# Kernel optimization log

Hardware: AMD Instinct MI355X
Metric: run time of the kernel (lower is better)

Reference implementation:

```python
import jax, jax.numpy as jnp
import numpy as np

BETA = 2.0  # config.beta_start (beta_anneal=True, step 0)


def _generate_e8_roots() -> np.ndarray:
    roots = []
    # 112 integer roots: (+-1, +-1, 0^6) in all index pairs
    for i in range(8):
        for j in range(i + 1, 8):
            for si in (1.0, -1.0):
                for sj in (1.0, -1.0):
                    v = np.zeros(8, dtype=np.float32)
                    v[i] = si
                    v[j] = sj
                    roots.append(v)
    # 128 half-integer roots: (+-1/2)^8 with even number of minus signs
    for bits in range(256):
        signs = np.array([1.0 if ((bits >> k) & 1) == 0 else -1.0 for k in range(8)], dtype=np.float32)
        if int((signs < 0).sum()) % 2 == 0:
            roots.append(0.5 * signs)
    return np.stack(roots)  # [240, 8], each of norm sqrt(2)


def setup_inputs() -> dict:
    key = jax.random.key(0)
    ks = jax.random.split(key, 4)
    B, S, D_Q, H, D_K, N_SLOTS, D_V = 4, 65536, 14, 32, 8, 240, 256
    query = jax.random.normal(ks[0], (B, S, D_Q), dtype=jnp.float32)
    # orthogonal-ish init approximated with scaled gaussians (math path identical)
    W1 = jax.random.normal(ks[1], (H, D_Q), dtype=jnp.float32) * (1.0 / np.sqrt(D_Q))
    b1 = jnp.zeros((H,), dtype=jnp.float32)
    W2 = jax.random.normal(ks[2], (D_K, H), dtype=jnp.float32) * (1.0 / np.sqrt(H))
    b2 = jnp.zeros((D_K,), dtype=jnp.float32)
    values = jax.random.normal(ks[3], (N_SLOTS, D_V), dtype=jnp.float32) * 0.02
    roots = _generate_e8_roots()
    keys_n = jnp.asarray(roots / np.linalg.norm(roots, axis=-1, keepdims=True))
    return {"query": query, "W1": W1, "b1": b1, "W2": W2, "b2": b2,
            "values": values, "keys_n": keys_n}


def reference(query, W1, b1, W2, b2, values, keys_n):
    # flatten [B,S,D] -> [N,D] as in read()
    x = query.reshape(-1, query.shape[-1])
    # G2Projection: Linear(14,32) -> GELU (exact) -> Linear(32,8) -> L2 normalize
    h = jax.nn.gelu(x @ W1.T + b1, approximate=False)
    q8 = h @ W2.T + b2
    q8 = q8 / jnp.maximum(jnp.linalg.norm(q8, axis=-1, keepdims=True), 1e-12)
    # Hopfield attention over 240 normalized E8 root keys
    sim = q8 @ keys_n.T                      # [N, 240]
    attn = jax.nn.softmax(BETA * sim, axis=-1)
    content = attn @ values                  # [N, 256]
    return content, attn
```

## Files before the change

### kernel.cpp

```cpp
#include <hip/hip_runtime.h>
#include <math.h>

#define DQ 14
#define HD 32
#define DK 8
#define NK 240
#define DV 256
#define RB 64
#define NFRAG 65536

typedef __attribute__((ext_vector_type(8))) short bf16x8;
typedef __attribute__((ext_vector_type(4))) float f32x4;

__device__ __forceinline__ unsigned bf16_rn(float x) {
    unsigned u = __float_as_uint(x);
    return (u + 0x7fffu + ((u >> 16) & 1u)) >> 16;
}

__global__ void prep_values(const float* __restrict__ values,
                            unsigned short* __restrict__ ws_hi,
                            unsigned short* __restrict__ ws_lo) {
    int idx = blockIdx.x * 256 + threadIdx.x;
    int e  = idx & 7;
    int l  = (idx >> 3) & 63;
    int ks = (idx >> 9) & 7;
    int nt = idx >> 12;
    int k = ks * 32 + ((l >> 4) << 3) + e;
    int n = nt * 16 + (l & 15);
    float v = (k < NK) ? values[k * DV + n] : 0.0f;
    unsigned hb = bf16_rn(v);
    float hf = __uint_as_float(hb << 16);
    unsigned lb = bf16_rn(v - hf);
    ws_hi[idx] = (unsigned short)hb;
    ws_lo[idx] = (unsigned short)lb;
}

__global__ __launch_bounds__(256, 2)
void em_fused(const float* __restrict__ query,
              const float* __restrict__ W1, const float* __restrict__ b1,
              const float* __restrict__ W2, const float* __restrict__ b2,
              const float* __restrict__ keys,
              const unsigned short* __restrict__ ws_hi,
              const unsigned short* __restrict__ ws_lo,
              float* __restrict__ out_content, float* __restrict__ out_attn)
{
    __shared__ float s_x[RB][DQ];
    __shared__ float s_h[RB][HD + 1];
    __shared__ float s_q8[RB][DK + 1];
    __shared__ __align__(16) unsigned short s_Ah[RB * 256];
    __shared__ __align__(16) unsigned short s_Al[RB * 256];

    const int tid = threadIdx.x;
    const long row0 = (long)blockIdx.x * RB;

    for (int e = tid; e < RB * DQ; e += 256) {
        s_x[e / DQ][e % DQ] = query[row0 * DQ + e];
    }
    __syncthreads();

    #pragma unroll
    for (int it = 0; it < (RB * HD) / 256; ++it) {
        int task = it * 256 + tid;
        int r = task >> 5, j = task & 31;
        float acc = b1[j];
        #pragma unroll
        for (int c = 0; c < DQ; ++c) acc += s_x[r][c] * W1[j * DQ + c];
        s_h[r][j] = 0.5f * acc * (1.0f + erff(acc * 0.70710678118654752f));
    }
    __syncthreads();

    #pragma unroll
    for (int it = 0; it < (RB * DK) / 256; ++it) {
        int task = it * 256 + tid;
        int r = task >> 3, i = task & 7;
        float acc = b2[i];
        #pragma unroll
        for (int c = 0; c < HD; ++c) acc += s_h[r][c] * W2[i * HD + c];
        s_q8[r][i] = acc;
    }
    __syncthreads();

    if (tid < RB) {
        float ss = 0.f;
        #pragma unroll
        for (int i = 0; i < DK; ++i) { float v = s_q8[tid][i]; ss += v * v; }
        float inv = 1.0f / fmaxf(sqrtf(ss), 1e-12f);
        #pragma unroll
        for (int i = 0; i < DK; ++i) s_q8[tid][i] *= inv;
    }
    __syncthreads();

    {
        const int wv = tid >> 6, lane = tid & 63;
        const int t0 = lane * 4;
        float kr[4][DK];
        #pragma unroll
        for (int s = 0; s < 4; ++s) {
            #pragma unroll
            for (int c = 0; c < DK; ++c)
                kr[s][c] = (t0 + s < NK) ? keys[(t0 + s) * DK + c] : 0.0f;
        }
        char* ahp = (char*)s_Ah;
        char* alp = (char*)s_Al;
        for (int rr = 0; rr < 16; ++rr) {
            const int r = wv * 16 + rr;
            float q[DK];
            #pragma unroll
            for (int c = 0; c < DK; ++c) q[c] = s_q8[r][c];
            float ex[4];
            float ssum = 0.f;
            #pragma unroll
            for (int s = 0; s < 4; ++s) {
                float sim = 0.f;
                #pragma unroll
                for (int c = 0; c < DK; ++c) sim += q[c] * kr[s][c];
                float v = (t0 + s < NK) ? __expf(2.0f * sim) : 0.0f;
                ex[s] = v;
                ssum += v;
            }
            #pragma unroll
            for (int m = 1; m < 64; m <<= 1) ssum += __shfl_xor(ssum, m, 64);
            const float inv = 1.0f / ssum;
            float a0 = ex[0] * inv, a1 = ex[1] * inv, a2 = ex[2] * inv, a3 = ex[3] * inv;
            if (t0 < NK) {
                *(float4*)&out_attn[(row0 + r) * NK + t0] =
                    make_float4(a0, a1, a2, a3);
            }
            unsigned h0 = bf16_rn(a0), h1 = bf16_rn(a1), h2 = bf16_rn(a2), h3 = bf16_rn(a3);
            float f0 = __uint_as_float(h0 << 16), f1 = __uint_as_float(h1 << 16);
            float f2 = __uint_as_float(h2 << 16), f3 = __uint_as_float(h3 << 16);
            unsigned l0 = bf16_rn(a0 - f0), l1 = bf16_rn(a1 - f1);
            unsigned l2 = bf16_rn(a2 - f2), l3 = bf16_rn(a3 - f3);
            unsigned off = ((unsigned)(r * 512 + lane * 8)) ^ (((unsigned)(r & 7)) << 4);
            *(ushort4*)(ahp + off) = make_ushort4((unsigned short)h0, (unsigned short)h1,
                                                  (unsigned short)h2, (unsigned short)h3);
            *(ushort4*)(alp + off) = make_ushort4((unsigned short)l0, (unsigned short)l1,
                                                  (unsigned short)l2, (unsigned short)l3);
        }
    }
    __syncthreads();

    {
        const int wv = tid >> 6, lane = tid & 63;
        const int l15 = lane & 15, l4 = lane >> 4;
        f32x4 acc[4][4];
        #pragma unroll
        for (int i = 0; i < 4; ++i)
            #pragma unroll
            for (int j = 0; j < 4; ++j)
                acc[i][j] = (f32x4){0.f, 0.f, 0.f, 0.f};

        const char* ahp = (const char*)s_Ah;
        const char* alp = (const char*)s_Al;
        const bf16x8* Bh = (const bf16x8*)ws_hi;
        const bf16x8* Bl = (const bf16x8*)ws_lo;

        #pragma unroll
        for (int ks = 0; ks < 8; ++ks) {
            bf16x8 bh[4], bl[4], ah[4], al[4];
            #pragma unroll
            for (int ntl = 0; ntl < 4; ++ntl) {
                int fi = (((wv * 4 + ntl) * 8 + ks) << 6) + lane;
                bh[ntl] = Bh[fi];
                bl[ntl] = Bl[fi];
            }
            #pragma unroll
            for (int mt = 0; mt < 4; ++mt) {
                int m = mt * 16 + l15;
                unsigned off = ((unsigned)(m * 512 + ks * 64 + l4 * 16)) ^
                               (((unsigned)(m & 7)) << 4);
                ah[mt] = *(const bf16x8*)(ahp + off);
                al[mt] = *(const bf16x8*)(alp + off);
            }
            #pragma unroll
            for (int ntl = 0; ntl < 4; ++ntl) {
                #pragma unroll
                for (int mt = 0; mt < 4; ++mt) {
                    acc[mt][ntl] = __builtin_amdgcn_mfma_f32_16x16x32_bf16(
                        ah[mt], bh[ntl], acc[mt][ntl], 0, 0, 0);
                    acc[mt][ntl] = __builtin_amdgcn_mfma_f32_16x16x32_bf16(
                        al[mt], bh[ntl], acc[mt][ntl], 0, 0, 0);
                    acc[mt][ntl] = __builtin_amdgcn_mfma_f32_16x16x32_bf16(
                        ah[mt], bl[ntl], acc[mt][ntl], 0, 0, 0);
                }
            }
        }

        #pragma unroll
        for (int mt = 0; mt < 4; ++mt) {
            #pragma unroll
            for (int ntl = 0; ntl < 4; ++ntl) {
                const int n = (wv * 4 + ntl) * 16 + l15;
                #pragma unroll
                for (int j = 0; j < 4; ++j) {
                    long row = row0 + mt * 16 + l4 * 4 + j;
                    out_content[row * DV + n] = acc[mt][ntl][j];
                }
            }
        }
    }
}

extern "C" void kernel_launch(void* const* d_in, const int* in_sizes, int n_in,
                              void* d_out, int out_size, void* d_ws, size_t ws_size,
                              hipStream_t stream) {
    const float* query  = (const float*)d_in[0];
    const float* W1     = (const float*)d_in[1];
    const float* b1     = (const float*)d_in[2];
    const float* W2     = (const float*)d_in[3];
    const float* b2     = (const float*)d_in[4];
    const float* values = (const float*)d_in[5];
    const float* keys   = (const float*)d_in[6];

    const int nrows = in_sizes[0] / DQ;
    float* out_content = (float*)d_out;
    float* out_attn    = out_content + (size_t)nrows * DV;

    unsigned short* wh = (unsigned short*)d_ws;
    unsigned short* wl = wh + NFRAG;

    prep_values<<<NFRAG / 256, 256, 0, stream>>>(values, wh, wl);
    em_fused<<<nrows / RB, 256, 0, stream>>>(query, W1, b1, W2, b2, keys,
                                             wh, wl, out_content, out_attn);
}
```

Baseline: 732.0 us.

## Use 512-thread blocks and swap MFMA operands for vectorized content stores

```diff
diff --git a/kernel.cpp b/kernel.cpp
--- a/kernel.cpp
+++ b/kernel.cpp
@@ -7,6 +7,7 @@
 #define NK 240
 #define DV 256
 #define RB 64
+#define NT 512
 #define NFRAG 65536
 
 typedef __attribute__((ext_vector_type(8))) short bf16x8;
@@ -35,7 +36,7 @@
     ws_lo[idx] = (unsigned short)lb;
 }
 
-__global__ __launch_bounds__(256, 2)
+__global__ __launch_bounds__(NT, 4)
 void em_fused(const float* __restrict__ query,
               const float* __restrict__ W1, const float* __restrict__ b1,
               const float* __restrict__ W2, const float* __restrict__ b2,
@@ -53,14 +54,14 @@
     const int tid = threadIdx.x;
     const long row0 = (long)blockIdx.x * RB;
 
-    for (int e = tid; e < RB * DQ; e += 256) {
+    for (int e = tid; e < RB * DQ; e += NT) {
         s_x[e / DQ][e % DQ] = query[row0 * DQ + e];
     }
     __syncthreads();
 
     #pragma unroll
-    for (int it = 0; it < (RB * HD) / 256; ++it) {
-        int task = it * 256 + tid;
+    for (int it = 0; it < (RB * HD) / NT; ++it) {
+        int task = it * NT + tid;
         int r = task >> 5, j = task & 31;
         float acc = b1[j];
         #pragma unroll
@@ -69,10 +70,8 @@
     }
     __syncthreads();
 
-    #pragma unroll
-    for (int it = 0; it < (RB * DK) / 256; ++it) {
-        int task = it * 256 + tid;
-        int r = task >> 3, i = task & 7;
+    {
+        int r = tid >> 3, i = tid & 7;
         float acc = b2[i];
         #pragma unroll
         for (int c = 0; c < HD; ++c) acc += s_h[r][c] * W2[i * HD + c];
@@ -102,8 +101,8 @@
         }
         char* ahp = (char*)s_Ah;
         char* alp = (char*)s_Al;
-        for (int rr = 0; rr < 16; ++rr) {
-            const int r = wv * 16 + rr;
+        for (int rr = 0; rr < 8; ++rr) {
+            const int r = wv * 8 + rr;
             float q[DK];
             #pragma unroll
             for (int c = 0; c < DK; ++c) q[c] = s_q8[r][c];
@@ -143,26 +142,26 @@
     {
         const int wv = tid >> 6, lane = tid & 63;
         const int l15 = lane & 15, l4 = lane >> 4;
-        f32x4 acc[4][4];
+        f32x4 acc[4][2];
         #pragma unroll
         for (int i = 0; i < 4; ++i)
             #pragma unroll
-            for (int j = 0; j < 4; ++j)
+            for (int j = 0; j < 2; ++j)
                 acc[i][j] = (f32x4){0.f, 0.f, 0.f, 0.f};
 
         const char* ahp = (const char*)s_Ah;
         const char* alp = (const char*)s_Al;
-        const bf16x8* Bh = (const bf16x8*)ws_hi;
-        const bf16x8* Bl = (const bf16x8*)ws_lo;
+        const bf16x8* Vh = (const bf16x8*)ws_hi;
+        const bf16x8* Vl = (const bf16x8*)ws_lo;
 
         #pragma unroll
         for (int ks = 0; ks < 8; ++ks) {
-            bf16x8 bh[4], bl[4], ah[4], al[4];
-            #pragma unroll
-            for (int ntl = 0; ntl < 4; ++ntl) {
-                int fi = (((wv * 4 + ntl) * 8 + ks) << 6) + lane;
-                bh[ntl] = Bh[fi];
-                bl[ntl] = Bl[fi];
+            bf16x8 vh[2], vl[2], ah[4], al[4];
+            #pragma unroll
+            for (int ntl = 0; ntl < 2; ++ntl) {
+                int fi = (((wv * 2 + ntl) * 8 + ks) << 6) + lane;
+                vh[ntl] = Vh[fi];
+                vl[ntl] = Vl[fi];
             }
             #pragma unroll
             for (int mt = 0; mt < 4; ++mt) {
@@ -173,29 +172,28 @@
                 al[mt] = *(const bf16x8*)(alp + off);
             }
             #pragma unroll
-            for (int ntl = 0; ntl < 4; ++ntl) {
+            for (int ntl = 0; ntl < 2; ++ntl) {
                 #pragma unroll
                 for (int mt = 0; mt < 4; ++mt) {
                     acc[mt][ntl] = __builtin_amdgcn_mfma_f32_16x16x32_bf16(
-                        ah[mt], bh[ntl], acc[mt][ntl], 0, 0, 0);
+                        vh[ntl], ah[mt], acc[mt][ntl], 0, 0, 0);
                     acc[mt][ntl] = __builtin_amdgcn_mfma_f32_16x16x32_bf16(
-                        al[mt], bh[ntl], acc[mt][ntl], 0, 0, 0);
+                        vl[ntl], ah[mt], acc[mt][ntl], 0, 0, 0);
                     acc[mt][ntl] = __builtin_amdgcn_mfma_f32_16x16x32_bf16(
-                        ah[mt], bl[ntl], acc[mt][ntl], 0, 0, 0);
+                        vh[ntl], al[mt], acc[mt][ntl], 0, 0, 0);
                 }
             }
         }
 
         #pragma unroll
         for (int mt = 0; mt < 4; ++mt) {
-            #pragma unroll
-            for (int ntl = 0; ntl < 4; ++ntl) {
-                const int n = (wv * 4 + ntl) * 16 + l15;
-                #pragma unroll
-                for (int j = 0; j < 4; ++j) {
-                    long row = row0 + mt * 16 + l4 * 4 + j;
-                    out_content[row * DV + n] = acc[mt][ntl][j];
-                }
+            const long row = row0 + mt * 16 + l15;
+            #pragma unroll
+            for (int ntl = 0; ntl < 2; ++ntl) {
+                const int n = (wv * 2 + ntl) * 16 + l4 * 4;
+                float4 o = make_float4(acc[mt][ntl][0], acc[mt][ntl][1],
+                                       acc[mt][ntl][2], acc[mt][ntl][3]);
+                *(float4*)&out_content[row * DV + n] = o;
             }
         }
     }
@@ -220,6 +218,6 @@
     unsigned short* wl = wh + NFRAG;
 
     prep_values<<<NFRAG / 256, 256, 0, stream>>>(values, wh, wl);
-    em_fused<<<nrows / RB, 256, 0, stream>>>(query, W1, b1, W2, b2, keys,
-                                             wh, wl, out_content, out_attn);
-}
+    em_fused<<<nrows / RB, NT, 0, stream>>>(query, W1, b1, W2, b2, keys,
+                                            wh, wl, out_content, out_attn);
+}
```

Measured after the change: 697.9 us. 1.05x faster.
